# Performance work log

Measured on AMD Instinct MI355X. Metric: run time of the kernel, lower is better.

## Reference

```python
import jax, jax.numpy as jnp
import numpy as np
import math

T, B, V, D = 8, 32, 50257, 256
N = 4096            # memory slots
H = 4               # attention heads
L = 2               # transformer layers
K = 3               # shift width
HALF = K // 2
WIN = 16            # controller window
RH, WH = 1, 1       # read / write heads
EPS = 1e-12


def _pe(win, d):
    pos = jnp.arange(win, dtype=jnp.float32)[:, None]
    div = jnp.exp(jnp.arange(0, d, 2, dtype=jnp.float32) * (-math.log(10000.0) / d))
    pe = jnp.zeros((win, d), dtype=jnp.float32)
    pe = pe.at[:, 0::2].set(jnp.sin(pos * div))
    pe = pe.at[:, 1::2].set(jnp.cos(pos * div))
    return pe[:, None, :]


def _ln(x, g, b, eps=1e-5):
    mu = x.mean(-1, keepdims=True)
    var = ((x - mu) ** 2).mean(-1, keepdims=True)
    return (x - mu) * jax.lax.rsqrt(var + eps) * g + b


def _mha(x, Wqkv, bqkv, Wo, bo):
    S, Bc, Dm = x.shape
    dh = Dm // H
    qkv = x @ Wqkv.T + bqkv
    q, k, v = jnp.split(qkv, 3, axis=-1)
    q = q.reshape(S, Bc, H, dh)
    k = k.reshape(S, Bc, H, dh)
    v = v.reshape(S, Bc, H, dh)
    logits = jnp.einsum('sbhd,tbhd->bhst', q, k) / math.sqrt(dh)
    a = jax.nn.softmax(logits, axis=-1)
    o = jnp.einsum('bhst,tbhd->sbhd', a, v).reshape(S, Bc, Dm)
    return o @ Wo.T + bo


def _addressing(key_v, beta, gate, shift, gamma, prev_w, memory):
    # key_v [B,M], beta/gate/gamma [B,1], shift [B,K], prev_w [B,N], memory [B,N,M]
    key_n = key_v / (jnp.linalg.norm(key_v, axis=-1, keepdims=True) + EPS)
    mem_n = memory / (jnp.linalg.norm(memory, axis=-1, keepdims=True) + EPS)
    cos = jnp.einsum('bnm,bm->bn', mem_n, key_n)
    wc = jax.nn.softmax(jax.nn.softplus(beta) * cos, axis=-1)
    g = jax.nn.sigmoid(gate)
    wg = g * wc + (1.0 - g) * prev_w
    s = jax.nn.softmax(shift, axis=-1)
    shifted = sum(s[:, k:k + 1] * jnp.roll(wg, k - HALF, axis=-1) for k in range(K))
    gp = 1.0 + jax.nn.softplus(gamma)
    wt = (shifted + EPS) ** gp
    return wt / (wt.sum(-1, keepdims=True) + EPS)


def setup_inputs() -> dict:
    key = jax.random.key(0)
    ks = iter(jax.random.split(key, 40))
    def w(shape, s=0.02):
        return jax.random.normal(next(ks), shape, jnp.float32) * s
    return {
        'tokens': jax.random.randint(next(ks), (T, B), 0, V, jnp.int32),
        'emb_W': w((V, D)),
        'read_gate_W': w((D, D)), 'read_gate_b': jnp.zeros((D,)),
        'film_W': w((2 * D, D)), 'film_b': jnp.zeros((2 * D,)),
        't_Wqkv': w((L, 3 * D, D)), 't_bqkv': jnp.zeros((L, 3 * D)),
        't_Wo': w((L, D, D)), 't_bo': jnp.zeros((L, D)),
        't_ln1_g': jnp.ones((L, D)), 't_ln1_b': jnp.zeros((L, D)),
        't_ln2_g': jnp.ones((L, D)), 't_ln2_b': jnp.zeros((L, D)),
        't_W1': w((L, 4 * D, D)), 't_b1': jnp.zeros((L, 4 * D)),
        't_W2': w((L, D, 4 * D)), 't_b2': jnp.zeros((L, D)),
        'out_ln_g': jnp.ones((D,)), 'out_ln_b': jnp.zeros((D,)),
        'lstm_Wih': w((2, 4 * D, D)), 'lstm_Whh': w((2, 4 * D, D)),
        'lstm_bih': jnp.zeros((2, 4 * D)), 'lstm_bhh': jnp.zeros((2, 4 * D)),
        'head_W': w((V, D)), 'head_b': jnp.zeros((V,)),
        'read_W': w((D + 3 + K, D)), 'read_b': jnp.zeros((D + 3 + K,)),
        'write_W': w((3 * D + 3 + K, D)), 'write_b': jnp.zeros((3 * D + 3 + K,)),
    }


def reference(tokens, emb_W, read_gate_W, read_gate_b, film_W, film_b,
              t_Wqkv, t_bqkv, t_Wo, t_bo, t_ln1_g, t_ln1_b, t_ln2_g, t_ln2_b,
              t_W1, t_b1, t_W2, t_b2, out_ln_g, out_ln_b,
              lstm_Wih, lstm_Whh, lstm_bih, lstm_bhh,
              head_W, head_b, read_W, read_b, write_W, write_b):
    pe = _pe(WIN, D)
    memory = jnp.zeros((B, N, D), jnp.float32)
    read_w = jnp.zeros((B, RH, N), jnp.float32).at[:, :, 0].set(1.0)
    write_w = jnp.zeros((B, WH, N), jnp.float32).at[:, :, 0].set(1.0)
    record = jnp.zeros((B, D), jnp.float32)
    hx = jnp.zeros((2, B, D), jnp.float32)
    cx = jnp.zeros((2, B, D), jnp.float32)
    hist = jnp.zeros((1, B, D), jnp.float32)
    logits_all = []
    for t in range(T):  # T fixed, sequential recurrence (context length grows)
        emb = emb_W[tokens[t]]                               # [B,D]
        r = jnp.einsum('bhn,bnm->bm', read_w, memory)        # sum over read heads
        fp = record @ film_W.T + film_b
        gam = 1.0 + jnp.tanh(fp[:, :D])
        bet = fp[:, D:]
        rg = jax.nn.sigmoid(record @ read_gate_W.T + read_gate_b)
        x_in = gam * emb + bet + rg * r
        ctx = jnp.concatenate([hist, x_in[None]], axis=0)
        if ctx.shape[0] > WIN:
            ctx = ctx[-WIN:]
        hist = ctx
        h = ctx + pe[:ctx.shape[0]]
        for l in range(L):  # norm_first pre-LN encoder layers (eval, relu FFN)
            h = h + _mha(_ln(h, t_ln1_g[l], t_ln1_b[l]), t_Wqkv[l], t_bqkv[l], t_Wo[l], t_bo[l])
            h = h + (jax.nn.relu(_ln(h, t_ln2_g[l], t_ln2_b[l]) @ t_W1[l].T + t_b1[l]) @ t_W2[l].T + t_b2[l])
        c_out = _ln(h[-1], out_ln_g, out_ln_b)
        # 2-layer LSTM single step (torch gate order i,f,g,o)
        x_l = c_out
        new_h, new_c = [], []
        for l in range(2):
            gates = x_l @ lstm_Wih[l].T + lstm_bih[l] + hx[l] @ lstm_Whh[l].T + lstm_bhh[l]
            i_g, f_g, g_g, o_g = jnp.split(gates, 4, axis=-1)
            c_new = jax.nn.sigmoid(f_g) * cx[l] + jax.nn.sigmoid(i_g) * jnp.tanh(g_g)
            h_new = jax.nn.sigmoid(o_g) * jnp.tanh(c_new)
            new_h.append(h_new); new_c.append(c_new)
            x_l = h_new
        hx = jnp.stack(new_h); cx = jnp.stack(new_c)
        record = hx[-1]
        c_out = c_out + x_l
        logits_all.append(c_out @ head_W.T + head_b)
        # read addressing
        rp = (c_out @ read_W.T + read_b).reshape(B, RH, -1)
        new_rw = []
        for hh in range(RH):
            p = rp[:, hh]
            new_rw.append(_addressing(p[:, :D], p[:, D:D + 1], p[:, D + 1:D + 2],
                                      p[:, D + 2:D + 2 + K], p[:, D + 2 + K:D + 3 + K],
                                      read_w[:, hh], memory))
        read_w = jnp.stack(new_rw, axis=1)
        # write addressing + erase/add (addressing uses pre-update memory)
        wp = (c_out @ write_W.T + write_b).reshape(B, WH, -1)
        mem_pre = memory
        new_ww = []
        for hh in range(WH):
            p = wp[:, hh]
            wt = _addressing(p[:, :D], p[:, D:D + 1], p[:, D + 1:D + 2],
                             p[:, D + 2:D + 2 + K], p[:, D + 2 + K:D + 3 + K],
                             write_w[:, hh], mem_pre)
            erase = jax.nn.sigmoid(p[:, D + 3 + K:2 * D + 3 + K])
            add = jnp.tanh(p[:, 2 * D + 3 + K:3 * D + 3 + K])
            memory = memory * (1.0 - wt[:, :, None] * erase[:, None, :]) + wt[:, :, None] * add[:, None, :]
            new_ww.append(wt)
        write_w = jnp.stack(new_ww, axis=1)
    return jnp.stack(logits_all, axis=0)  # [T, B, V]
```

## Files before the change

kernel.cpp:

```cpp
#include <hip/hip_runtime.h>
#include <math.h>

#define TT 8
#define BB 32
#define VV 50257
#define DD 256
#define NN 4096
#define EPS_ 1e-12f

typedef __attribute__((ext_vector_type(8))) short short8;
typedef __attribute__((ext_vector_type(4))) float f32x4;

__device__ __forceinline__ float sigf(float x) { return 1.f / (1.f + expf(-x)); }
__device__ __forceinline__ float softplusf_(float x) { return fmaxf(x, 0.f) + log1pf(expf(-fabsf(x))); }
__device__ __forceinline__ unsigned f2bf(float f) {
  union { float f; unsigned u; } c; c.f = f;
  return (c.u + 0x7FFFu + ((c.u >> 16) & 1u)) >> 16;
}
__device__ __forceinline__ float bf2f(unsigned u16) {
  union { unsigned u; float f; } c; c.u = u16 << 16; return c.f;
}

__device__ __forceinline__ float blk_sum(float v, float* s) {
#pragma unroll
  for (int o = 32; o > 0; o >>= 1) v += __shfl_down(v, o);
  __syncthreads();
  if ((threadIdx.x & 63) == 0) s[threadIdx.x >> 6] = v;
  __syncthreads();
  return s[0] + s[1] + s[2] + s[3];
}
__device__ __forceinline__ float blk_max(float v, float* s) {
#pragma unroll
  for (int o = 32; o > 0; o >>= 1) v = fmaxf(v, __shfl_down(v, o));
  __syncthreads();
  if ((threadIdx.x & 63) == 0) s[threadIdx.x >> 6] = v;
  __syncthreads();
  return fmaxf(fmaxf(s[0], s[1]), fmaxf(s[2], s[3]));
}

__global__ void init_k(float* rw, float* ww, float* hpe) {
  int i = blockIdx.x * 256 + threadIdx.x;
  if (i < BB) { rw[(size_t)i * NN] = 1.f; ww[(size_t)i * NN] = 1.f; }
  if (i < BB * DD) hpe[i] = (i & 1) ? 1.f : 0.f;
}

__global__ void cvtw_k(const float* __restrict__ W, unsigned short* __restrict__ Wh, int n4) {
  int i = blockIdx.x * 256 + threadIdx.x;
  if (i >= n4) return;
  float4 v = *(const float4*)(W + (size_t)i * 4);
  uint2 p;
  p.x = f2bf(v.x) | (f2bf(v.y) << 16);
  p.y = f2bf(v.z) | (f2bf(v.w) << 16);
  *(uint2*)(Wh + (size_t)i * 4) = p;
}

__global__ void catlstm_k(const float* __restrict__ Wih, const float* __restrict__ Whh,
                          const float* __restrict__ bih, const float* __restrict__ bhh,
                          unsigned short* __restrict__ Wc, float* __restrict__ cb) {
  int i = blockIdx.x * 256 + threadIdx.x;
  if (i >= 2 * 1024 * 512) return;
  int k = i & 511, np = (i >> 9) & 1023, l = i >> 19;
  int d = np >> 2, gate = np & 3;
  int src = gate * 256 + d;
  float v = (k < 256) ? Wih[((size_t)l * 1024 + src) * 256 + k]
                      : Whh[((size_t)l * 1024 + src) * 256 + (k - 256)];
  Wc[i] = (unsigned short)f2bf(v);
  if (k == 0) cb[l * 1024 + np] = bih[l * 1024 + src] + bhh[l * 1024 + src];
}

__global__ void catrw_k(const float* __restrict__ rW, const float* __restrict__ rb,
                        const float* __restrict__ wW, const float* __restrict__ wb,
                        unsigned short* __restrict__ Wrw, float* __restrict__ brw) {
  int i = blockIdx.x * 256 + threadIdx.x;
  if (i >= 1036 * 256) return;
  int k = i & 255, n = i >> 8;
  float v = (n < 262) ? rW[(size_t)n * 256 + k] : wW[(size_t)(n - 262) * 256 + k];
  Wrw[i] = (unsigned short)f2bf(v);
  if (k == 0) brw[n] = (n < 262) ? rb[n] : wb[n - 262];
}

__global__ void brc_k(const float* __restrict__ fb, const float* __restrict__ rb, float* __restrict__ brc) {
  int i = blockIdx.x * 256 + threadIdx.x;
  if (i < 512) brc[i] = fb[i];
  else if (i < 768) brc[i] = rb[i - 512];
}

__global__ __launch_bounds__(256) void ln0_k(const float* __restrict__ hpe,
                                             const float* __restrict__ g1, const float* __restrict__ b1,
                                             unsigned short* __restrict__ q1b) {
  __shared__ float s8[8];
  int b = blockIdx.x, d = threadIdx.x;
  float v = hpe[(size_t)b * 256 + d];
  float mu = blk_sum(v, s8) * (1.f / 256.f);
  float dd = v - mu;
  float var = blk_sum(dd * dd, s8) * (1.f / 256.f);
  float rs = rsqrtf(var + 1e-5f);
  q1b[(size_t)b * 256 + d] = (unsigned short)f2bf(dd * rs * g1[d] + b1[d]);
}

template <int EPI>
__global__ __launch_bounds__(256) void gA_k(const unsigned short* __restrict__ A,
                                            const unsigned short* __restrict__ W,
                                            const float* __restrict__ bias,
                                            float* __restrict__ Cf,
                                            unsigned short* __restrict__ Cb,
                                            int ldc, int Nlim) {
  const int tid = threadIdx.x, w = tid >> 6, l = tid & 63, r = l & 15, q = l >> 4;
  const int m0 = blockIdx.y * 32;
  const int n = blockIdx.x * 64 + w * 16 + r;
  const unsigned short* Ap = A + (size_t)m0 * 256;
  const unsigned short* Wp = W + (size_t)n * 256;
  f32x4 acc0 = {0.f, 0.f, 0.f, 0.f}, acc1 = {0.f, 0.f, 0.f, 0.f};
#pragma unroll
  for (int kt = 0; kt < 8; ++kt) {
    short8 a0 = *(const short8*)(Ap + r * 256 + kt * 32 + q * 8);
    short8 a1 = *(const short8*)(Ap + (16 + r) * 256 + kt * 32 + q * 8);
    short8 bf = *(const short8*)(Wp + kt * 32 + q * 8);
    acc0 = __builtin_amdgcn_mfma_f32_16x16x32_bf16(a0, bf, acc0, 0, 0, 0);
    acc1 = __builtin_amdgcn_mfma_f32_16x16x32_bf16(a1, bf, acc1, 0, 0, 0);
  }
  if (n >= Nlim) return;
  float bb = bias[n];
#pragma unroll
  for (int e = 0; e < 4; ++e) {
    int m1 = m0 + q * 4 + e, m2 = m1 + 16;
    float v1 = acc0[e] + bb, v2 = acc1[e] + bb;
    if constexpr (EPI == 0) {
      Cf[(size_t)m1 * ldc + n] = v1;
      Cf[(size_t)m2 * ldc + n] = v2;
    } else {
      Cb[(size_t)m1 * ldc + n] = (unsigned short)f2bf(fmaxf(v1, 0.f));
      Cb[(size_t)m2 * ldc + n] = (unsigned short)f2bf(fmaxf(v2, 0.f));
    }
  }
}

template <int K, int OLN>
__global__ __launch_bounds__(256) void gB_k(const unsigned short* __restrict__ A,
                                            const unsigned short* __restrict__ W,
                                            const float* __restrict__ bias,
                                            const float* __restrict__ resid,
                                            float* __restrict__ Hout,
                                            const float* __restrict__ lng,
                                            const float* __restrict__ lnb,
                                            unsigned short* __restrict__ Xb, int xstride,
                                            float* __restrict__ c_out) {
  __shared__ float hv[32][260];
  const int tid = threadIdx.x, w = tid >> 6, l = tid & 63, r = l & 15, q = l >> 4;
  const int m0 = blockIdx.x * 32;
  const unsigned short* Ap = A + (size_t)m0 * K;
  const unsigned short* Wp0 = W + (size_t)(w * 64 + 0 + r) * K;
  const unsigned short* Wp1 = W + (size_t)(w * 64 + 16 + r) * K;
  const unsigned short* Wp2 = W + (size_t)(w * 64 + 32 + r) * K;
  const unsigned short* Wp3 = W + (size_t)(w * 64 + 48 + r) * K;
  f32x4 acc0[4], acc1[4];
#pragma unroll
  for (int j = 0; j < 4; ++j) { acc0[j] = {0.f, 0.f, 0.f, 0.f}; acc1[j] = {0.f, 0.f, 0.f, 0.f}; }
#pragma unroll 4
  for (int kt = 0; kt < K / 32; ++kt) {
    short8 a0 = *(const short8*)(Ap + (size_t)r * K + kt * 32 + q * 8);
    short8 a1 = *(const short8*)(Ap + (size_t)(16 + r) * K + kt * 32 + q * 8);
    short8 b0 = *(const short8*)(Wp0 + kt * 32 + q * 8);
    short8 b1 = *(const short8*)(Wp1 + kt * 32 + q * 8);
    short8 b2 = *(const short8*)(Wp2 + kt * 32 + q * 8);
    short8 b3 = *(const short8*)(Wp3 + kt * 32 + q * 8);
    acc0[0] = __builtin_amdgcn_mfma_f32_16x16x32_bf16(a0, b0, acc0[0], 0, 0, 0);
    acc1[0] = __builtin_amdgcn_mfma_f32_16x16x32_bf16(a1, b0, acc1[0], 0, 0, 0);
    acc0[1] = __builtin_amdgcn_mfma_f32_16x16x32_bf16(a0, b1, acc0[1], 0, 0, 0);
    acc1[1] = __builtin_amdgcn_mfma_f32_16x16x32_bf16(a1, b1, acc1[1], 0, 0, 0);
    acc0[2] = __builtin_amdgcn_mfma_f32_16x16x32_bf16(a0, b2, acc0[2], 0, 0, 0);
    acc1[2] = __builtin_amdgcn_mfma_f32_16x16x32_bf16(a1, b2, acc1[2], 0, 0, 0);
    acc0[3] = __builtin_amdgcn_mfma_f32_16x16x32_bf16(a0, b3, acc0[3], 0, 0, 0);
    acc1[3] = __builtin_amdgcn_mfma_f32_16x16x32_bf16(a1, b3, acc1[3], 0, 0, 0);
  }
#pragma unroll
  for (int j = 0; j < 4; ++j) {
    int n = w * 64 + j * 16 + r;
    float bb = bias[n];
#pragma unroll
    for (int e = 0; e < 4; ++e) {
      int m1 = q * 4 + e, m2 = m1 + 16;
      float v1 = acc0[j][e] + bb + resid[(size_t)(m0 + m1) * 256 + n];
      float v2 = acc1[j][e] + bb + resid[(size_t)(m0 + m2) * 256 + n];
      Hout[(size_t)(m0 + m1) * 256 + n] = v1;
      Hout[(size_t)(m0 + m2) * 256 + n] = v2;
      hv[m1][n] = v1;
      hv[m2][n] = v2;
    }
  }
  __syncthreads();
  const float4 g4 = *(const float4*)(lng + l * 4);
  const float4 be4 = *(const float4*)(lnb + l * 4);
#pragma unroll
  for (int i = 0; i < 8; ++i) {
    int row = w * 8 + i;
    float4 v = *(const float4*)&hv[row][l * 4];
    float s1 = v.x + v.y + v.z + v.w;
    float s2 = v.x * v.x + v.y * v.y + v.z * v.z + v.w * v.w;
#pragma unroll
    for (int o = 32; o > 0; o >>= 1) { s1 += __shfl_xor(s1, o); s2 += __shfl_xor(s2, o); }
    float mu = s1 * (1.f / 256.f);
    float var = fmaxf(s2 * (1.f / 256.f) - mu * mu, 0.f);
    float rs = rsqrtf(var + 1e-5f);
    float y0 = (v.x - mu) * rs * g4.x + be4.x;
    float y1 = (v.y - mu) * rs * g4.y + be4.y;
    float y2 = (v.z - mu) * rs * g4.z + be4.z;
    float y3 = (v.w - mu) * rs * g4.w + be4.w;
    uint2 pk;
    pk.x = f2bf(y0) | (f2bf(y1) << 16);
    pk.y = f2bf(y2) | (f2bf(y3) << 16);
    *(uint2*)(Xb + (size_t)(m0 + row) * xstride + l * 4) = pk;
    if constexpr (OLN) {
      float4 cv = make_float4(y0, y1, y2, y3);
      *(float4*)(c_out + (size_t)(m0 + row) * 256 + l * 4) = cv;
    }
  }
}

template <int LAST>
__global__ __launch_bounds__(256) void gL_k(const unsigned short* __restrict__ A,
                                            const unsigned short* __restrict__ W,
                                            const float* __restrict__ cbias,
                                            float* __restrict__ cx,
                                            unsigned short* __restrict__ li_own,
                                            unsigned short* __restrict__ li_next,
                                            const float* __restrict__ c_outp,
                                            unsigned short* __restrict__ cfinb,
                                            unsigned short* __restrict__ record_b) {
  __shared__ float g[32][68];
  const int tid = threadIdx.x, w = tid >> 6, l = tid & 63, r = l & 15, q = l >> 4;
  const int n = blockIdx.x * 64 + w * 16 + r;
  const unsigned short* Wp = W + (size_t)n * 512;
  f32x4 acc0 = {0.f, 0.f, 0.f, 0.f}, acc1 = {0.f, 0.f, 0.f, 0.f};
#pragma unroll 4
  for (int kt = 0; kt < 16; ++kt) {
    short8 a0 = *(const short8*)(A + (size_t)r * 512 + kt * 32 + q * 8);
    short8 a1 = *(const short8*)(A + (size_t)(16 + r) * 512 + kt * 32 + q * 8);
    short8 bf = *(const short8*)(Wp + kt * 32 + q * 8);
    acc0 = __builtin_amdgcn_mfma_f32_16x16x32_bf16(a0, bf, acc0, 0, 0, 0);
    acc1 = __builtin_amdgcn_mfma_f32_16x16x32_bf16(a1, bf, acc1, 0, 0, 0);
  }
  float bb = cbias[n];
  int nb = w * 16 + r;
#pragma unroll
  for (int e = 0; e < 4; ++e) {
    g[q * 4 + e][nb] = acc0[e] + bb;
    g[16 + q * 4 + e][nb] = acc1[e] + bb;
  }
  __syncthreads();
#pragma unroll
  for (int h2 = 0; h2 < 2; ++h2) {
    int u = tid + 256 * h2;
    int b = u >> 4, dd = u & 15;
    int dg = blockIdx.x * 16 + dd;
    float gi = g[b][dd * 4 + 0], gf = g[b][dd * 4 + 1];
    float gg = g[b][dd * 4 + 2], go = g[b][dd * 4 + 3];
    float c = sigf(gf) * cx[b * 256 + dg] + sigf(gi) * tanhf(gg);
    float hN = sigf(go) * tanhf(c);
    cx[b * 256 + dg] = c;
    li_own[(size_t)b * 512 + 256 + dg] = (unsigned short)f2bf(hN);
    if constexpr (LAST) {
      record_b[b * 256 + dg] = (unsigned short)f2bf(hN);
      cfinb[b * 256 + dg] = (unsigned short)f2bf(c_outp[b * 256 + dg] + hN);
    } else {
      li_next[(size_t)b * 512 + dg] = (unsigned short)f2bf(hN);
    }
  }
}

__global__ __launch_bounds__(256) void xinpw_k(const int* __restrict__ tokens,
                                               const float* __restrict__ embW,
                                               const float* __restrict__ fp,
                                               const float* __restrict__ rvec,
                                               const float* __restrict__ g1, const float* __restrict__ b1,
                                               float* __restrict__ hpe,
                                               unsigned short* __restrict__ q1b, int t) {
  __shared__ float s8[8];
  int b = blockIdx.x, d = threadIdx.x;
  float gam = 1.f + tanhf(fp[(size_t)b * 768 + d]);
  float bet = fp[(size_t)b * 768 + 256 + d];
  float rg = sigf(fp[(size_t)b * 768 + 512 + d]);
  int tok = tokens[t * BB + b];
  float emb = embW[(size_t)tok * 256 + d];
  float ang = (float)(t + 1) * expf(-logf(10000.f) * (float)(d & ~1) / 256.f);
  float pe = (d & 1) ? cosf(ang) : sinf(ang);
  float x = gam * emb + bet + rg * rvec[b * 256 + d] + pe;
  hpe[((size_t)(t + 1) * BB + b) * 256 + d] = x;
  float mu = blk_sum(x, s8) * (1.f / 256.f);
  float dd = x - mu;
  float var = blk_sum(dd * dd, s8) * (1.f / 256.f);
  float rs = rsqrtf(var + 1e-5f);
  q1b[((size_t)(t + 1) * BB + b) * 256 + d] = (unsigned short)f2bf(dd * rs * g1[d] + b1[d]);
}

__global__ __launch_bounds__(128) void attn_k(const float* __restrict__ qkv,
                                              unsigned short* __restrict__ ao, int S) {
  int bh = blockIdx.x;
  int b = bh >> 2, h = bh & 3;
  __shared__ float q[9][64], k[9][64], v[9][64], lg[9][12];
  int tid = threadIdx.x;
  for (int i = tid; i < S * 64; i += 128) {
    int s = i >> 6, d = i & 63;
    const float* base = qkv + (size_t)(s * BB + b) * 768 + h * 64 + d;
    q[s][d] = base[0]; k[s][d] = base[256]; v[s][d] = base[512];
  }
  __syncthreads();
  for (int p = tid; p < S * S; p += 128) {
    int s = p / S, t2 = p % S;
    float acc = 0.f;
    for (int d = 0; d < 64; ++d) acc += q[s][d] * k[t2][d];
    lg[s][t2] = acc * 0.125f;
  }
  __syncthreads();
  if (tid < S) {
    float mx = -1e30f;
    for (int t2 = 0; t2 < S; ++t2) mx = fmaxf(mx, lg[tid][t2]);
    float sum = 0.f;
    for (int t2 = 0; t2 < S; ++t2) { float e = expf(lg[tid][t2] - mx); lg[tid][t2] = e; sum += e; }
    float inv = 1.f / sum;
    for (int t2 = 0; t2 < S; ++t2) lg[tid][t2] *= inv;
  }
  __syncthreads();
  for (int i = tid; i < S * 64; i += 128) {
    int s = i >> 6, d = i & 63;
    float o = 0.f;
    for (int t2 = 0; t2 < S; ++t2) o += lg[s][t2] * v[t2][d];
    ao[(size_t)(s * BB + b) * 256 + h * 64 + d] = (unsigned short)f2bf(o);
  }
}

__global__ __launch_bounds__(64) void attnl_k(const float* __restrict__ qkv,
                                              unsigned short* __restrict__ ao, int S) {
  int bh = blockIdx.x;
  int b = bh >> 2, h = bh & 3;
  int d = threadIdx.x;
  __shared__ float sc[9];
  float qd = qkv[(size_t)((S - 1) * BB + b) * 768 + h * 64 + d];
  for (int j = 0; j < S; ++j) {
    float p = qd * qkv[(size_t)(j * BB + b) * 768 + h * 64 + 256 + d];
#pragma unroll
    for (int o = 32; o > 0; o >>= 1) p += __shfl_down(p, o);
    if (d == 0) sc[j] = p * 0.125f;
  }
  __syncthreads();
  float mx = -1e30f;
  for (int j = 0; j < S; ++j) mx = fmaxf(mx, sc[j]);
  float pj[9], sum = 0.f;
  for (int j = 0; j < S; ++j) { pj[j] = expf(sc[j] - mx); sum += pj[j]; }
  float inv = 1.f / sum;
  float o = 0.f;
  for (int j = 0; j < S; ++j) o += pj[j] * inv * qkv[(size_t)(j * BB + b) * 768 + h * 64 + 512 + d];
  ao[(size_t)b * 256 + h * 64 + d] = (unsigned short)f2bf(o);
}

__global__ __launch_bounds__(256) void head_k(const unsigned short* __restrict__ Wh,
                                              const unsigned short* __restrict__ Ah,
                                              const float* __restrict__ hb,
                                              float* __restrict__ out) {
  const int tid = threadIdx.x;
  const int w = tid >> 6, l = tid & 63;
  const int r = l & 15, q = l >> 4;
  const int n = blockIdx.x * 64 + w * 16 + r;
  const int nc = n < VV ? n : VV - 1;
  const short* Ap = (const short*)Ah;
  const short* Wp = (const short*)Wh + (size_t)nc * 256;
  short8 a0[8], a1[8], bf[8];
#pragma unroll
  for (int kt = 0; kt < 8; ++kt) {
    a0[kt] = *(const short8*)(Ap + r * 256 + kt * 32 + q * 8);
    a1[kt] = *(const short8*)(Ap + (16 + r) * 256 + kt * 32 + q * 8);
    bf[kt] = *(const short8*)(Wp + kt * 32 + q * 8);
  }
  f32x4 acc0 = {0.f, 0.f, 0.f, 0.f}, acc1 = {0.f, 0.f, 0.f, 0.f};
#pragma unroll
  for (int kt = 0; kt < 8; ++kt) {
    acc0 = __builtin_amdgcn_mfma_f32_16x16x32_bf16(a0[kt], bf[kt], acc0, 0, 0, 0);
    acc1 = __builtin_amdgcn_mfma_f32_16x16x32_bf16(a1[kt], bf[kt], acc1, 0, 0, 0);
  }
  if (n < VV) {
    float bb = hb[n];
#pragma unroll
    for (int e = 0; e < 4; ++e) {
      int m = q * 4 + e;
      out[(size_t)m * VV + n] = acc0[e] + bb;
      out[(size_t)(16 + m) * VV + n] = acc1[e] + bb;
    }
  }
}

__global__ __launch_bounds__(256) void passA_k(const unsigned short* __restrict__ mem,
                                               const float* __restrict__ rpwp,
                                               float* __restrict__ dr,
                                               float* __restrict__ dw,
                                               float* __restrict__ nrm) {
  __shared__ float kr[256], kw[256];
  int b = blockIdx.y, tid = threadIdx.x;
  kr[tid] = rpwp[(size_t)b * 1036 + tid];
  kw[tid] = rpwp[(size_t)b * 1036 + 262 + tid];
  __syncthreads();
  int w = tid >> 6, lane = tid & 63;
  float4 kr4 = *(float4*)&kr[lane * 4];
  float4 kw4 = *(float4*)&kw[lane * 4];
  int n0 = blockIdx.x * 16 + w * 4;
  for (int rr = 0; rr < 4; ++rr) {
    int n = n0 + rr;
    const unsigned short* row = mem + ((size_t)b * NN + n) * 256;
    uint2 p = *(const uint2*)(row + lane * 4);
    float m0 = bf2f(p.x & 0xffffu), m1 = bf2f(p.x >> 16);
    float m2 = bf2f(p.y & 0xffffu), m3 = bf2f(p.y >> 16);
    float pr = m0 * kr4.x + m1 * kr4.y + m2 * kr4.z + m3 * kr4.w;
    float pw = m0 * kw4.x + m1 * kw4.y + m2 * kw4.z + m3 * kw4.w;
    float pn = m0 * m0 + m1 * m1 + m2 * m2 + m3 * m3;
#pragma unroll
    for (int o = 32; o > 0; o >>= 1) {
      pr += __shfl_down(pr, o); pw += __shfl_down(pw, o); pn += __shfl_down(pn, o);
    }
    if (lane == 0) {
      dr[(size_t)b * NN + n] = pr;
      dw[(size_t)b * NN + n] = pw;
      nrm[(size_t)b * NN + n] = pn;
    }
  }
}

__global__ __launch_bounds__(256) void addr_k(const float* __restrict__ dr,
                                              const float* __restrict__ dw,
                                              const float* __restrict__ nrm,
                                              const float* __restrict__ rpwp,
                                              float* rw, float* ww,
                                              float* __restrict__ ea,
                                              float* __restrict__ rvec) {
  __shared__ float wg[4096];
  __shared__ float s8[8];
  int head = blockIdx.x & 1, b = blockIdx.x >> 1;
  int tid = threadIdx.x;
  const float* p = rpwp + (size_t)b * 1036 + (head ? 262 : 0);
  const float* dot = (head ? dw : dr) + (size_t)b * NN;
  const float* n2 = nrm + (size_t)b * NN;
  float* wout = (head ? ww : rw) + (size_t)b * NN;

  float kv = p[tid];
  float kn = sqrtf(blk_sum(kv * kv, s8)) + EPS_;
  float beta = p[256], gate = p[257], sh0 = p[258], sh1 = p[259], sh2 = p[260], gamma = p[261];
  float spb = softplusf_(beta);
  float g = sigf(gate);
  float mx3 = fmaxf(sh0, fmaxf(sh1, sh2));
  float e0 = expf(sh0 - mx3), e1 = expf(sh1 - mx3), e2 = expf(sh2 - mx3);
  float esum = e0 + e1 + e2;
  float s0 = e0 / esum, s1 = e1 / esum, s2 = e2 / esum;
  float gp = 1.f + softplusf_(gamma);

  float l[16];
  float lmax = -1e30f;
#pragma unroll
  for (int i = 0; i < 16; ++i) {
    int n = tid + i * 256;
    float cs = dot[n] / ((sqrtf(n2[n]) + EPS_) * kn);
    l[i] = spb * cs;
    lmax = fmaxf(lmax, l[i]);
  }
  float Mx = blk_max(lmax, s8);
  float es = 0.f;
#pragma unroll
  for (int i = 0; i < 16; ++i) { l[i] = expf(l[i] - Mx); es += l[i]; }
  float SS = blk_sum(es, s8);
  float inv = 1.f / SS;
#pragma unroll
  for (int i = 0; i < 16; ++i) {
    int n = tid + i * 256;
    wg[n] = g * l[i] * inv + (1.f - g) * wout[n];
  }
  __syncthreads();
  float wt[16];
  float wsum = 0.f;
#pragma unroll
  for (int i = 0; i < 16; ++i) {
    int n = tid + i * 256;
    float sh = s0 * wg[(n + 1) & 4095] + s1 * wg[n] + s2 * wg[(n + 4095) & 4095];
    wt[i] = powf(sh + EPS_, gp);
    wsum += wt[i];
  }
  float WS = blk_sum(wsum, s8) + EPS_;
  float winv = 1.f / WS;
#pragma unroll
  for (int i = 0; i < 16; ++i) wout[tid + i * 256] = wt[i] * winv;

  if (head) {
    ea[(size_t)b * 512 + tid] = sigf(p[262 + tid]);
    ea[(size_t)b * 512 + 256 + tid] = tanhf(p[518 + tid]);
  } else {
    rvec[(size_t)b * 256 + tid] = 0.f;
  }
}

template <int FIRST>
__global__ __launch_bounds__(256) void passB_k(unsigned short* mem, const float* __restrict__ ww,
                                               const float* __restrict__ rw,
                                               const float* __restrict__ ea,
                                               float* __restrict__ rvec) {
  __shared__ float eS[256], aS[256];
  __shared__ float rred[4][256];
  int b = blockIdx.y, tid = threadIdx.x;
  eS[tid] = ea[(size_t)b * 512 + tid];
  aS[tid] = ea[(size_t)b * 512 + 256 + tid];
  __syncthreads();
  int w = tid >> 6, lane = tid & 63;
  float4 e4 = *(float4*)&eS[lane * 4];
  float4 a4 = *(float4*)&aS[lane * 4];
  float4 racc = make_float4(0.f, 0.f, 0.f, 0.f);
  int n0 = blockIdx.x * 128 + w * 32;
  for (int rr = 0; rr < 32; ++rr) {
    int n = n0 + rr;
    float wt = ww[(size_t)b * NN + n];
    float rwv = rw[(size_t)b * NN + n];
    unsigned short* row = mem + ((size_t)b * NN + n) * 256;
    float m0, m1, m2, m3;
    if (FIRST) {
      m0 = wt * a4.x; m1 = wt * a4.y; m2 = wt * a4.z; m3 = wt * a4.w;
    } else {
      uint2 p = *(const uint2*)(row + lane * 4);
      m0 = bf2f(p.x & 0xffffu) * (1.f - wt * e4.x) + wt * a4.x;
      m1 = bf2f(p.x >> 16) * (1.f - wt * e4.y) + wt * a4.y;
      m2 = bf2f(p.y & 0xffffu) * (1.f - wt * e4.z) + wt * a4.z;
      m3 = bf2f(p.y >> 16) * (1.f - wt * e4.w) + wt * a4.w;
    }
    uint2 pk;
    pk.x = f2bf(m0) | (f2bf(m1) << 16);
    pk.y = f2bf(m2) | (f2bf(m3) << 16);
    *(uint2*)(row + lane * 4) = pk;
    racc.x += rwv * m0; racc.y += rwv * m1; racc.z += rwv * m2; racc.w += rwv * m3;
  }
  rred[w][lane * 4 + 0] = racc.x;
  rred[w][lane * 4 + 1] = racc.y;
  rred[w][lane * 4 + 2] = racc.z;
  rred[w][lane * 4 + 3] = racc.w;
  __syncthreads();
  float s = rred[0][tid] + rred[1][tid] + rred[2][tid] + rred[3][tid];
  atomicAdd(rvec + (size_t)b * 256 + tid, s);
}

extern "C" void kernel_launch(void* const* d_in, const int* in_sizes, int n_in,
                              void* d_out, int out_size, void* d_ws, size_t ws_size,
                              hipStream_t stream) {
  const int* tokens = (const int*)d_in[0];
  const float* emb_W = (const float*)d_in[1];
  const float* read_gate_W = (const float*)d_in[2];
  const float* read_gate_b = (const float*)d_in[3];
  const float* film_W = (const float*)d_in[4];
  const float* film_b = (const float*)d_in[5];
  const float* t_Wqkv = (const float*)d_in[6];
  const float* t_bqkv = (const float*)d_in[7];
  const float* t_Wo = (const float*)d_in[8];
  const float* t_bo = (const float*)d_in[9];
  const float* t_ln1_g = (const float*)d_in[10];
  const float* t_ln1_b = (const float*)d_in[11];
  const float* t_ln2_g = (const float*)d_in[12];
  const float* t_ln2_b = (const float*)d_in[13];
  const float* t_W1 = (const float*)d_in[14];
  const float* t_b1 = (const float*)d_in[15];
  const float* t_W2 = (const float*)d_in[16];
  const float* t_b2 = (const float*)d_in[17];
  const float* out_ln_g = (const float*)d_in[18];
  const float* out_ln_b = (const float*)d_in[19];
  const float* lstm_Wih = (const float*)d_in[20];
  const float* lstm_Whh = (const float*)d_in[21];
  const float* lstm_bih = (const float*)d_in[22];
  const float* lstm_bhh = (const float*)d_in[23];
  const float* head_W = (const float*)d_in[24];
  const float* head_b = (const float*)d_in[25];
  const float* read_W = (const float*)d_in[26];
  const float* read_b = (const float*)d_in[27];
  const float* write_W = (const float*)d_in[28];
  const float* write_b = (const float*)d_in[29];
  float* out = (float*)d_out;

  float* ws = (float*)d_ws;
  size_t off = 0;
  float* read_w = ws + off; off += (size_t)BB * NN;
  float* write_w = ws + off; off += (size_t)BB * NN;
  float* cx = ws + off; off += 2 * BB * DD;
  float* r_vec = ws + off; off += BB * DD;
  float* dot_r = ws + off; off += (size_t)BB * NN;
  float* dot_w = ws + off; off += (size_t)BB * NN;
  float* norm2 = ws + off; off += (size_t)BB * NN;
  unsigned short* record_b = (unsigned short*)(ws + off); off += BB * DD / 2;
  unsigned short* lstm_in_b = (unsigned short*)(ws + off); off += 2 * BB * 512 / 2;
  size_t zero_floats = off;
  unsigned short* memory = (unsigned short*)(ws + off); off += (size_t)BB * NN * DD / 2;
  float* hpe = ws + off; off += 9 * BB * DD;
  float* h = ws + off; off += 9 * BB * DD;
  float* h2 = ws + off; off += BB * DD;
  float* qkvC = ws + off; off += 9 * BB * 768;
  float* qkv2 = ws + off; off += 9 * BB * 768;
  float* fp = ws + off; off += BB * 768;
  float* c_out = ws + off; off += BB * DD;
  float* rpwp = ws + off; off += BB * 1036;
  float* ea = ws + off; off += BB * 2 * DD;
  unsigned short* q1b = (unsigned short*)(ws + off); off += 9 * BB * DD / 2;
  unsigned short* q2b = (unsigned short*)(ws + off); off += 9 * BB * DD / 2;
  unsigned short* x2b = (unsigned short*)(ws + off); off += 9 * BB * DD / 2;
  unsigned short* x2b2 = (unsigned short*)(ws + off); off += BB * DD / 2;
  unsigned short* ao_b = (unsigned short*)(ws + off); off += 9 * BB * DD / 2;
  unsigned short* ao2_b = (unsigned short*)(ws + off); off += BB * DD / 2;
  unsigned short* mid_b = (unsigned short*)(ws + off); off += 9 * BB * 1024 / 2;
  unsigned short* cfinb = (unsigned short*)(ws + off); off += BB * DD / 2;
  unsigned short* Wh = (unsigned short*)(ws + off); off += (size_t)VV * 256 / 2;
  unsigned short* Wq_b = (unsigned short*)(ws + off); off += 2 * 768 * 256 / 2;
  unsigned short* Wo_b = (unsigned short*)(ws + off); off += 2 * 256 * 256 / 2;
  unsigned short* W1_b = (unsigned short*)(ws + off); off += 2 * 1024 * 256 / 2;
  unsigned short* W2_b = (unsigned short*)(ws + off); off += 2 * 256 * 1024 / 2;
  unsigned short* Wc_b = (unsigned short*)(ws + off); off += 2 * 1024 * 512 / 2;
  unsigned short* Wrw_b = (unsigned short*)(ws + off); off += 1088 * 256 / 2;
  unsigned short* FR_b = (unsigned short*)(ws + off); off += 768 * 256 / 2;
  float* cb2 = ws + off; off += 2 * 1024;
  float* brw = ws + off; off += 1040;
  float* brc = ws + off; off += 768;
  if (ws_size < off * sizeof(float)) return;

  (void)hipMemsetAsync(ws, 0, zero_floats * sizeof(float), stream);
  (void)hipMemsetAsync(Wrw_b + (size_t)1036 * 256, 0, (size_t)52 * 256 * 2, stream);
  init_k<<<32, 256, 0, stream>>>(read_w, write_w, hpe);
  cvtw_k<<<(VV * 256 / 4 + 255) / 256, 256, 0, stream>>>(head_W, Wh, VV * 256 / 4);
  cvtw_k<<<(2 * 768 * 256 / 4 + 255) / 256, 256, 0, stream>>>(t_Wqkv, Wq_b, 2 * 768 * 256 / 4);
  cvtw_k<<<(2 * 256 * 256 / 4 + 255) / 256, 256, 0, stream>>>(t_Wo, Wo_b, 2 * 256 * 256 / 4);
  cvtw_k<<<(2 * 1024 * 256 / 4 + 255) / 256, 256, 0, stream>>>(t_W1, W1_b, 2 * 1024 * 256 / 4);
  cvtw_k<<<(2 * 256 * 1024 / 4 + 255) / 256, 256, 0, stream>>>(t_W2, W2_b, 2 * 256 * 1024 / 4);
  cvtw_k<<<(512 * 256 / 4 + 255) / 256, 256, 0, stream>>>(film_W, FR_b, 512 * 256 / 4);
  cvtw_k<<<(256 * 256 / 4 + 255) / 256, 256, 0, stream>>>(read_gate_W, FR_b + 512 * 256, 256 * 256 / 4);
  catlstm_k<<<4096, 256, 0, stream>>>(lstm_Wih, lstm_Whh, lstm_bih, lstm_bhh, Wc_b, cb2);
  catrw_k<<<1036, 256, 0, stream>>>(read_W, read_b, write_W, write_b, Wrw_b, brw);
  brc_k<<<3, 256, 0, stream>>>(film_b, read_gate_b, brc);
  ln0_k<<<BB, 256, 0, stream>>>(hpe, t_ln1_g, t_ln1_b, q1b);
  gA_k<0><<<dim3(12, 1), 256, 0, stream>>>(q1b, Wq_b, t_bqkv, qkvC, nullptr, 768, 768);

  for (int t = 0; t < TT; ++t) {
    const int S = t + 2;

    gA_k<0><<<dim3(12, 1), 256, 0, stream>>>(record_b, FR_b, brc, fp, nullptr, 768, 768);
    xinpw_k<<<BB, 256, 0, stream>>>(tokens, emb_W, fp, r_vec, t_ln1_g, t_ln1_b, hpe, q1b, t);
    gA_k<0><<<dim3(12, 1), 256, 0, stream>>>(q1b + (size_t)(t + 1) * BB * 256, Wq_b, t_bqkv,
                                             qkvC + (size_t)(t + 1) * BB * 768, nullptr, 768, 768);
    attn_k<<<BB * 4, 128, 0, stream>>>(qkvC, ao_b, S);
    gB_k<256, 0><<<S, 256, 0, stream>>>(ao_b, Wo_b, t_bo, hpe, h, t_ln2_g, t_ln2_b, x2b, 256, nullptr);
    gA_k<1><<<dim3(16, S), 256, 0, stream>>>(x2b, W1_b, t_b1, nullptr, mid_b, 1024, 1024);
    gB_k<1024, 0><<<S, 256, 0, stream>>>(mid_b, W2_b, t_b2, h, h, t_ln1_g + 256, t_ln1_b + 256, q2b, 256, nullptr);

    gA_k<0><<<dim3(12, S), 256, 0, stream>>>(q2b, Wq_b + 768 * 256, t_bqkv + 768, qkv2, nullptr, 768, 768);
    attnl_k<<<BB * 4, 64, 0, stream>>>(qkv2, ao2_b, S);
    gB_k<256, 0><<<1, 256, 0, stream>>>(ao2_b, Wo_b + 256 * 256, t_bo + 256, h + (size_t)(S - 1) * BB * 256,
                                        h2, t_ln2_g + 256, t_ln2_b + 256, x2b2, 256, nullptr);
    gA_k<1><<<dim3(16, 1), 256, 0, stream>>>(x2b2, W1_b + 1024 * 256, t_b1 + 1024, nullptr, mid_b, 1024, 1024);
    gB_k<1024, 1><<<1, 256, 0, stream>>>(mid_b, W2_b + 256 * 1024, t_b2 + 256, h2, h2,
                                         out_ln_g, out_ln_b, lstm_in_b, 512, c_out);

    gL_k<0><<<16, 256, 0, stream>>>(lstm_in_b, Wc_b, cb2, cx, lstm_in_b, lstm_in_b + BB * 512,
                                    nullptr, nullptr, nullptr);
    gL_k<1><<<16, 256, 0, stream>>>(lstm_in_b + BB * 512, Wc_b + (size_t)1024 * 512, cb2 + 1024,
                                    cx + BB * DD, lstm_in_b + BB * 512, nullptr, c_out, cfinb, record_b);

    head_k<<<(VV + 63) / 64, 256, 0, stream>>>(Wh, cfinb, head_b, out + (size_t)t * BB * VV);

    if (t < TT - 1) {
      gA_k<0><<<dim3(17, 1), 256, 0, stream>>>(cfinb, Wrw_b, brw, rpwp, nullptr, 1036, 1036);
      if (t > 0)
        passA_k<<<dim3(NN / 16, BB), 256, 0, stream>>>(memory, rpwp, dot_r, dot_w, norm2);
      addr_k<<<2 * BB, 256, 0, stream>>>(dot_r, dot_w, norm2, rpwp, read_w, write_w, ea, r_vec);
      if (t == 0)
        passB_k<1><<<dim3(NN / 128, BB), 256, 0, stream>>>(memory, write_w, read_w, ea, r_vec);
      else
        passB_k<0><<<dim3(NN / 128, BB), 256, 0, stream>>>(memory, write_w, read_w, ea, r_vec);
    }
  }
}
```

Measured before the change: 1.679 ms.

## Fuse attention into output-projection GEMM and merge aux GEMMs into head kernel

Attention (both full and last-row variants) is computed inside a new kernel that immediately performs the Wo projection, residual add and LayerNorm, removing the separate attention kernels and their bf16 intermediate buffers. The read/write-parameter GEMM and the next step's FiLM/read-gate GEMM are folded into extra blocks of the vocab head kernel, so they run alongside it rather than as separate launches. This cuts several launches per timestep. In exchange, the fused attention is recomputed per block with more register pressure, and the extra blocks add a little tail work to the head kernel.

```diff
diff --git a/kernel.cpp b/kernel.cpp
--- a/kernel.cpp
+++ b/kernel.cpp
@@ -96,6 +96,32 @@
   float var = blk_sum(dd * dd, s8) * (1.f / 256.f);
   float rs = rsqrtf(var + 1e-5f);
   q1b[(size_t)b * 256 + d] = (unsigned short)f2bf(dd * rs * g1[d] + b1[d]);
+}
+
+__device__ __forceinline__ void gA_dev(const unsigned short* __restrict__ A,
+                                       const unsigned short* __restrict__ W,
+                                       const float* __restrict__ bias,
+                                       float* __restrict__ Cf, int ldc, int Nlim, int nblk) {
+  const int tid = threadIdx.x, w = tid >> 6, l = tid & 63, r = l & 15, q = l >> 4;
+  const int n = nblk * 64 + w * 16 + r;
+  const unsigned short* Wp = W + (size_t)n * 256;
+  f32x4 acc0 = {0.f, 0.f, 0.f, 0.f}, acc1 = {0.f, 0.f, 0.f, 0.f};
+#pragma unroll
+  for (int kt = 0; kt < 8; ++kt) {
+    short8 a0 = *(const short8*)(A + r * 256 + kt * 32 + q * 8);
+    short8 a1 = *(const short8*)(A + (16 + r) * 256 + kt * 32 + q * 8);
+    short8 bf = *(const short8*)(Wp + kt * 32 + q * 8);
+    acc0 = __builtin_amdgcn_mfma_f32_16x16x32_bf16(a0, bf, acc0, 0, 0, 0);
+    acc1 = __builtin_amdgcn_mfma_f32_16x16x32_bf16(a1, bf, acc1, 0, 0, 0);
+  }
+  if (n >= Nlim) return;
+  float bb = bias[n];
+#pragma unroll
+  for (int e = 0; e < 4; ++e) {
+    int m1 = q * 4 + e, m2 = m1 + 16;
+    Cf[(size_t)m1 * ldc + n] = acc0[e] + bb;
+    Cf[(size_t)m2 * ldc + n] = acc1[e] + bb;
+  }
 }
 
 template <int EPI>
@@ -214,6 +240,123 @@
       float4 cv = make_float4(y0, y1, y2, y3);
       *(float4*)(c_out + (size_t)(m0 + row) * 256 + l * 4) = cv;
     }
+  }
+}
+
+template <int LASTONLY>
+__global__ __launch_bounds__(256) void gBatt_k(const float* __restrict__ qkvsrc,
+                                               const unsigned short* __restrict__ W,
+                                               const float* __restrict__ bias,
+                                               const float* __restrict__ resid,
+                                               float* __restrict__ Hout,
+                                               const float* __restrict__ lng,
+                                               const float* __restrict__ lnb,
+                                               unsigned short* __restrict__ Xb, int S) {
+  __shared__ float hv[32][260];
+  __shared__ unsigned short Abf[32][264];
+  const int tid = threadIdx.x, w = tid >> 6, l = tid & 63, r = l & 15, q = l >> 4;
+  const int s = LASTONLY ? S - 1 : (int)blockIdx.x;
+  const int m0 = LASTONLY ? 0 : s * 32;
+  {
+    const int pid = tid >> 1, half = tid & 1;
+    const int b = pid >> 2, hh = pid & 3;
+    const float* qrow = qkvsrc + (size_t)(s * BB + b) * 768 + hh * 64 + half * 32;
+    float qv[32];
+#pragma unroll
+    for (int j = 0; j < 32; ++j) qv[j] = qrow[j];
+    float lg[9];
+#pragma unroll
+    for (int t2 = 0; t2 < 9; ++t2) {
+      if (t2 >= S) break;
+      const float* krow = qkvsrc + (size_t)(t2 * BB + b) * 768 + 256 + hh * 64 + half * 32;
+      float p = 0.f;
+#pragma unroll
+      for (int j = 0; j < 32; ++j) p += qv[j] * krow[j];
+      p += __shfl_xor(p, 1);
+      lg[t2] = p * 0.125f;
+    }
+    float mx = -1e30f;
+#pragma unroll
+    for (int t2 = 0; t2 < 9; ++t2) { if (t2 >= S) break; mx = fmaxf(mx, lg[t2]); }
+    float sm = 0.f;
+#pragma unroll
+    for (int t2 = 0; t2 < 9; ++t2) { if (t2 >= S) break; float e = expf(lg[t2] - mx); lg[t2] = e; sm += e; }
+    float inv = 1.f / sm;
+    float o[32] = {};
+#pragma unroll
+    for (int t2 = 0; t2 < 9; ++t2) {
+      if (t2 >= S) break;
+      const float* vrow = qkvsrc + (size_t)(t2 * BB + b) * 768 + 512 + hh * 64 + half * 32;
+      float pp = lg[t2] * inv;
+#pragma unroll
+      for (int j = 0; j < 32; ++j) o[j] += pp * vrow[j];
+    }
+#pragma unroll
+    for (int j = 0; j < 32; ++j)
+      Abf[b][hh * 64 + half * 32 + j] = (unsigned short)f2bf(o[j]);
+  }
+  __syncthreads();
+  const unsigned short* Wp0 = W + (size_t)(w * 64 + 0 + r) * 256;
+  const unsigned short* Wp1 = W + (size_t)(w * 64 + 16 + r) * 256;
+  const unsigned short* Wp2 = W + (size_t)(w * 64 + 32 + r) * 256;
+  const unsigned short* Wp3 = W + (size_t)(w * 64 + 48 + r) * 256;
+  f32x4 acc0[4], acc1[4];
+#pragma unroll
+  for (int j = 0; j < 4; ++j) { acc0[j] = {0.f, 0.f, 0.f, 0.f}; acc1[j] = {0.f, 0.f, 0.f, 0.f}; }
+#pragma unroll
+  for (int kt = 0; kt < 8; ++kt) {
+    short8 a0 = *(const short8*)(&Abf[r][kt * 32 + q * 8]);
+    short8 a1 = *(const short8*)(&Abf[16 + r][kt * 32 + q * 8]);
+    short8 b0 = *(const short8*)(Wp0 + kt * 32 + q * 8);
+    short8 b1 = *(const short8*)(Wp1 + kt * 32 + q * 8);
+    short8 b2 = *(const short8*)(Wp2 + kt * 32 + q * 8);
+    short8 b3 = *(const short8*)(Wp3 + kt * 32 + q * 8);
+    acc0[0] = __builtin_amdgcn_mfma_f32_16x16x32_bf16(a0, b0, acc0[0], 0, 0, 0);
+    acc1[0] = __builtin_amdgcn_mfma_f32_16x16x32_bf16(a1, b0, acc1[0], 0, 0, 0);
+    acc0[1] = __builtin_amdgcn_mfma_f32_16x16x32_bf16(a0, b1, acc0[1], 0, 0, 0);
+    acc1[1] = __builtin_amdgcn_mfma_f32_16x16x32_bf16(a1, b1, acc1[1], 0, 0, 0);
+    acc0[2] = __builtin_amdgcn_mfma_f32_16x16x32_bf16(a0, b2, acc0[2], 0, 0, 0);
+    acc1[2] = __builtin_amdgcn_mfma_f32_16x16x32_bf16(a1, b2, acc1[2], 0, 0, 0);
+    acc0[3] = __builtin_amdgcn_mfma_f32_16x16x32_bf16(a0, b3, acc0[3], 0, 0, 0);
+    acc1[3] = __builtin_amdgcn_mfma_f32_16x16x32_bf16(a1, b3, acc1[3], 0, 0, 0);
+  }
+#pragma unroll
+  for (int j = 0; j < 4; ++j) {
+    int n = w * 64 + j * 16 + r;
+    float bb = bias[n];
+#pragma unroll
+    for (int e = 0; e < 4; ++e) {
+      int m1 = q * 4 + e, m2 = m1 + 16;
+      float v1 = acc0[j][e] + bb + resid[(size_t)(m0 + m1) * 256 + n];
+      float v2 = acc1[j][e] + bb + resid[(size_t)(m0 + m2) * 256 + n];
+      Hout[(size_t)(m0 + m1) * 256 + n] = v1;
+      Hout[(size_t)(m0 + m2) * 256 + n] = v2;
+      hv[m1][n] = v1;
+      hv[m2][n] = v2;
+    }
+  }
+  __syncthreads();
+  const float4 g4 = *(const float4*)(lng + l * 4);
+  const float4 be4 = *(const float4*)(lnb + l * 4);
+#pragma unroll
+  for (int i = 0; i < 8; ++i) {
+    int row = w * 8 + i;
+    float4 v = *(const float4*)&hv[row][l * 4];
+    float s1 = v.x + v.y + v.z + v.w;
+    float s2 = v.x * v.x + v.y * v.y + v.z * v.z + v.w * v.w;
+#pragma unroll
+    for (int o = 32; o > 0; o >>= 1) { s1 += __shfl_xor(s1, o); s2 += __shfl_xor(s2, o); }
+    float mu = s1 * (1.f / 256.f);
+    float var = fmaxf(s2 * (1.f / 256.f) - mu * mu, 0.f);
+    float rs = rsqrtf(var + 1e-5f);
+    float y0 = (v.x - mu) * rs * g4.x + be4.x;
+    float y1 = (v.y - mu) * rs * g4.y + be4.y;
+    float y2 = (v.z - mu) * rs * g4.z + be4.z;
+    float y3 = (v.w - mu) * rs * g4.w + be4.w;
+    uint2 pk;
+    pk.x = f2bf(y0) | (f2bf(y1) << 16);
+    pk.y = f2bf(y2) | (f2bf(y3) << 16);
+    *(uint2*)(Xb + (size_t)(m0 + row) * 256 + l * 4) = pk;
   }
 }
 
@@ -293,74 +436,29 @@
   q1b[((size_t)(t + 1) * BB + b) * 256 + d] = (unsigned short)f2bf(dd * rs * g1[d] + b1[d]);
 }
 
-__global__ __launch_bounds__(128) void attn_k(const float* __restrict__ qkv,
-                                              unsigned short* __restrict__ ao, int S) {
-  int bh = blockIdx.x;
-  int b = bh >> 2, h = bh & 3;
-  __shared__ float q[9][64], k[9][64], v[9][64], lg[9][12];
-  int tid = threadIdx.x;
-  for (int i = tid; i < S * 64; i += 128) {
-    int s = i >> 6, d = i & 63;
-    const float* base = qkv + (size_t)(s * BB + b) * 768 + h * 64 + d;
-    q[s][d] = base[0]; k[s][d] = base[256]; v[s][d] = base[512];
-  }
-  __syncthreads();
-  for (int p = tid; p < S * S; p += 128) {
-    int s = p / S, t2 = p % S;
-    float acc = 0.f;
-    for (int d = 0; d < 64; ++d) acc += q[s][d] * k[t2][d];
-    lg[s][t2] = acc * 0.125f;
-  }
-  __syncthreads();
-  if (tid < S) {
-    float mx = -1e30f;
-    for (int t2 = 0; t2 < S; ++t2) mx = fmaxf(mx, lg[tid][t2]);
-    float sum = 0.f;
-    for (int t2 = 0; t2 < S; ++t2) { float e = expf(lg[tid][t2] - mx); lg[tid][t2] = e; sum += e; }
-    float inv = 1.f / sum;
-    for (int t2 = 0; t2 < S; ++t2) lg[tid][t2] *= inv;
-  }
-  __syncthreads();
-  for (int i = tid; i < S * 64; i += 128) {
-    int s = i >> 6, d = i & 63;
-    float o = 0.f;
-    for (int t2 = 0; t2 < S; ++t2) o += lg[s][t2] * v[t2][d];
-    ao[(size_t)(s * BB + b) * 256 + h * 64 + d] = (unsigned short)f2bf(o);
-  }
-}
-
-__global__ __launch_bounds__(64) void attnl_k(const float* __restrict__ qkv,
-                                              unsigned short* __restrict__ ao, int S) {
-  int bh = blockIdx.x;
-  int b = bh >> 2, h = bh & 3;
-  int d = threadIdx.x;
-  __shared__ float sc[9];
-  float qd = qkv[(size_t)((S - 1) * BB + b) * 768 + h * 64 + d];
-  for (int j = 0; j < S; ++j) {
-    float p = qd * qkv[(size_t)(j * BB + b) * 768 + h * 64 + 256 + d];
-#pragma unroll
-    for (int o = 32; o > 0; o >>= 1) p += __shfl_down(p, o);
-    if (d == 0) sc[j] = p * 0.125f;
-  }
-  __syncthreads();
-  float mx = -1e30f;
-  for (int j = 0; j < S; ++j) mx = fmaxf(mx, sc[j]);
-  float pj[9], sum = 0.f;
-  for (int j = 0; j < S; ++j) { pj[j] = expf(sc[j] - mx); sum += pj[j]; }
-  float inv = 1.f / sum;
-  float o = 0.f;
-  for (int j = 0; j < S; ++j) o += pj[j] * inv * qkv[(size_t)(j * BB + b) * 768 + h * 64 + 512 + d];
-  ao[(size_t)b * 256 + h * 64 + d] = (unsigned short)f2bf(o);
-}
-
-__global__ __launch_bounds__(256) void head_k(const unsigned short* __restrict__ Wh,
-                                              const unsigned short* __restrict__ Ah,
-                                              const float* __restrict__ hb,
-                                              float* __restrict__ out) {
+__global__ __launch_bounds__(256) void fusedHR_k(const unsigned short* __restrict__ Wh,
+                                                 const unsigned short* __restrict__ Ah,
+                                                 const float* __restrict__ hb,
+                                                 float* __restrict__ out,
+                                                 const unsigned short* __restrict__ Wrw,
+                                                 const float* __restrict__ brw,
+                                                 float* __restrict__ rpwp,
+                                                 const unsigned short* __restrict__ FRw,
+                                                 const float* __restrict__ brc,
+                                                 const unsigned short* __restrict__ record_b,
+                                                 float* __restrict__ fp,
+                                                 int do_aux) {
+  const int bid = blockIdx.x;
+  if (bid >= 786) {
+    if (!do_aux) return;
+    if (bid < 786 + 17) gA_dev(Ah, Wrw, brw, rpwp, 1036, 1036, bid - 786);
+    else gA_dev(record_b, FRw, brc, fp, 768, 768, bid - 803);
+    return;
+  }
   const int tid = threadIdx.x;
   const int w = tid >> 6, l = tid & 63;
   const int r = l & 15, q = l >> 4;
-  const int n = blockIdx.x * 64 + w * 16 + r;
+  const int n = bid * 64 + w * 16 + r;
   const int nc = n < VV ? n : VV - 1;
   const short* Ap = (const short*)Ah;
   const short* Wp = (const short*)Wh + (size_t)nc * 256;
@@ -600,8 +698,6 @@
   unsigned short* q2b = (unsigned short*)(ws + off); off += 9 * BB * DD / 2;
   unsigned short* x2b = (unsigned short*)(ws + off); off += 9 * BB * DD / 2;
   unsigned short* x2b2 = (unsigned short*)(ws + off); off += BB * DD / 2;
-  unsigned short* ao_b = (unsigned short*)(ws + off); off += 9 * BB * DD / 2;
-  unsigned short* ao2_b = (unsigned short*)(ws + off); off += BB * DD / 2;
   unsigned short* mid_b = (unsigned short*)(ws + off); off += 9 * BB * 1024 / 2;
   unsigned short* cfinb = (unsigned short*)(ws + off); off += BB * DD / 2;
   unsigned short* Wh = (unsigned short*)(ws + off); off += (size_t)VV * 256 / 2;
@@ -632,23 +728,22 @@
   brc_k<<<3, 256, 0, stream>>>(film_b, read_gate_b, brc);
   ln0_k<<<BB, 256, 0, stream>>>(hpe, t_ln1_g, t_ln1_b, q1b);
   gA_k<0><<<dim3(12, 1), 256, 0, stream>>>(q1b, Wq_b, t_bqkv, qkvC, nullptr, 768, 768);
+  gA_k<0><<<dim3(12, 1), 256, 0, stream>>>(record_b, FR_b, brc, fp, nullptr, 768, 768);
 
   for (int t = 0; t < TT; ++t) {
     const int S = t + 2;
 
-    gA_k<0><<<dim3(12, 1), 256, 0, stream>>>(record_b, FR_b, brc, fp, nullptr, 768, 768);
     xinpw_k<<<BB, 256, 0, stream>>>(tokens, emb_W, fp, r_vec, t_ln1_g, t_ln1_b, hpe, q1b, t);
     gA_k<0><<<dim3(12, 1), 256, 0, stream>>>(q1b + (size_t)(t + 1) * BB * 256, Wq_b, t_bqkv,
                                              qkvC + (size_t)(t + 1) * BB * 768, nullptr, 768, 768);
-    attn_k<<<BB * 4, 128, 0, stream>>>(qkvC, ao_b, S);
-    gB_k<256, 0><<<S, 256, 0, stream>>>(ao_b, Wo_b, t_bo, hpe, h, t_ln2_g, t_ln2_b, x2b, 256, nullptr);
+    gBatt_k<0><<<S, 256, 0, stream>>>(qkvC, Wo_b, t_bo, hpe, h, t_ln2_g, t_ln2_b, x2b, S);
     gA_k<1><<<dim3(16, S), 256, 0, stream>>>(x2b, W1_b, t_b1, nullptr, mid_b, 1024, 1024);
     gB_k<1024, 0><<<S, 256, 0, stream>>>(mid_b, W2_b, t_b2, h, h, t_ln1_g + 256, t_ln1_b + 256, q2b, 256, nullptr);
 
     gA_k<0><<<dim3(12, S), 256, 0, stream>>>(q2b, Wq_b + 768 * 256, t_bqkv + 768, qkv2, nullptr, 768, 768);
-    attnl_k<<<BB * 4, 64, 0, stream>>>(qkv2, ao2_b, S);
-    gB_k<256, 0><<<1, 256, 0, stream>>>(ao2_b, Wo_b + 256 * 256, t_bo + 256, h + (size_t)(S - 1) * BB * 256,
-                                        h2, t_ln2_g + 256, t_ln2_b + 256, x2b2, 256, nullptr);
+    gBatt_k<1><<<1, 256, 0, stream>>>(qkv2, Wo_b + 256 * 256, t_bo + 256,
+                                      h + (size_t)(S - 1) * BB * 256, h2,
+                                      t_ln2_g + 256, t_ln2_b + 256, x2b2, S);
     gA_k<1><<<dim3(16, 1), 256, 0, stream>>>(x2b2, W1_b + 1024 * 256, t_b1 + 1024, nullptr, mid_b, 1024, 1024);
     gB_k<1024, 1><<<1, 256, 0, stream>>>(mid_b, W2_b + 256 * 1024, t_b2 + 256, h2, h2,
                                          out_ln_g, out_ln_b, lstm_in_b, 512, c_out);
@@ -658,10 +753,10 @@
     gL_k<1><<<16, 256, 0, stream>>>(lstm_in_b + BB * 512, Wc_b + (size_t)1024 * 512, cb2 + 1024,
                                     cx + BB * DD, lstm_in_b + BB * 512, nullptr, c_out, cfinb, record_b);
 
-    head_k<<<(VV + 63) / 64, 256, 0, stream>>>(Wh, cfinb, head_b, out + (size_t)t * BB * VV);
+    fusedHR_k<<<815, 256, 0, stream>>>(Wh, cfinb, head_b, out + (size_t)t * BB * VV,
+                                       Wrw_b, brw, rpwp, FR_b, brc, record_b, fp, t < TT - 1);
 
     if (t < TT - 1) {
-      gA_k<0><<<dim3(17, 1), 256, 0, stream>>>(cfinb, Wrw_b, brw, rpwp, nullptr, 1036, 1036);
       if (t > 0)
         passA_k<<<dim3(NN / 16, BB), 256, 0, stream>>>(memory, rpwp, dot_r, dot_w, norm2);
       addr_k<<<2 * BB, 256, 0, stream>>>(dot_r, dot_w, norm2, rpwp, read_w, write_w, ea, r_vec);
```

New measurement: 1.698 ms. About the same (+1.1%).
